# Performance work log

Measured on AMD Instinct MI355X. Metric: run time of the kernel, lower is better.

The kernel has to match this reference:

```python
import jax, jax.numpy as jnp
import numpy as np

B, IMG, P, S, D, H, HD = 64, 224, 16, 197, 768, 12, 64
MLP, L, PRUNE_AFTER, NCLS = 3072, 12, 4, 1000
N_KEEP = max(1, int(S * 0.5))  # FIXED_RATIO = 0.5 -> 98 kept tokens (plus forced CLS)


def _ln(x, w, b, eps=1e-6):
    m = x.mean(-1, keepdims=True)
    v = ((x - m) ** 2).mean(-1, keepdims=True)
    return (x - m) * jax.lax.rsqrt(v + eps) * w + b


def _block(x, ln1_w, ln1_b, qkv_w, qkv_b, proj_w, proj_b,
           ln2_w, ln2_b, fc1_w, fc1_b, fc2_w, fc2_b, key_mask=None):
    b, s, _ = x.shape
    qkv = _ln(x, ln1_w, ln1_b) @ qkv_w.T + qkv_b           # [B,S,3D]
    qkv = qkv.reshape(b, s, 3, H, HD)
    q, k, v = qkv[:, :, 0], qkv[:, :, 1], qkv[:, :, 2]     # [B,S,H,HD]
    logits = jnp.einsum('bqhd,bkhd->bhqk', q * (HD ** -0.5), k)
    if key_mask is not None:
        # masking pruned keys == varlen attention restricted to kept tokens
        logits = jnp.where(key_mask[:, None, None, :], logits, -1e9)
    attn = jax.nn.softmax(logits, axis=-1)
    out = jnp.einsum('bhqk,bkhd->bqhd', attn, v).reshape(b, s, D)
    x = x + out @ proj_w.T + proj_b
    h = _ln(x, ln2_w, ln2_b)
    h = jax.nn.gelu(h @ fc1_w.T + fc1_b, approximate=False) @ fc2_w.T + fc2_b
    return x + h


def _forward(images, patch_w, patch_b, cls_token, pos_embed,
             ln1_w, ln1_b, qkv_w, qkv_b, proj_w, proj_b,
             ln2_w, ln2_b, fc1_w, fc1_b, fc2_w, fc2_b,
             norm_w, norm_b, head_w, head_b):
    # patch embed: conv stride P == non-overlapping patch projection
    x = jax.lax.conv_general_dilated(images, patch_w, (P, P), 'VALID',
                                     dimension_numbers=('NCHW', 'OIHW', 'NCHW'))
    x = x.reshape(x.shape[0], D, -1).transpose(0, 2, 1) + patch_b       # [B,196,D]
    x = jnp.concatenate([jnp.broadcast_to(cls_token, (x.shape[0], 1, D)), x], axis=1)
    x = x + pos_embed                                                    # [B,197,D]
    for i in range(PRUNE_AFTER):
        x = _block(x, ln1_w[i], ln1_b[i], qkv_w[i], qkv_b[i], proj_w[i], proj_b[i],
                   ln2_w[i], ln2_b[i], fc1_w[i], fc1_b[i], fc2_w[i], fc2_b[i])
    # norm-score topk prune (CLS always kept), as in _threshold_prune
    scores = jnp.linalg.norm(x, axis=-1)                                 # [B,S]
    _, idx = jax.lax.top_k(scores, N_KEEP)
    mask = jnp.zeros((x.shape[0], S), bool)
    mask = mask.at[jnp.arange(x.shape[0])[:, None], idx].set(True).at[:, 0].set(True)
    # Padded-mask form of triton_pack_tokens + flash_attn_varlen: pruned tokens
    # are never attended to (masked keys) and their own outputs are unused.
    for i in range(PRUNE_AFTER, L):
        x = _block(x, ln1_w[i], ln1_b[i], qkv_w[i], qkv_b[i], proj_w[i], proj_b[i],
                   ln2_w[i], ln2_b[i], fc1_w[i], fc1_b[i], fc2_w[i], fc2_b[i],
                   key_mask=mask)
    cls = _ln(x[:, 0], norm_w, norm_b)   # packed[cu[:-1]] is always the CLS token
    return cls @ head_w.T + head_b       # [B, NCLS]


def setup_inputs():
    key = jax.random.key(0)
    ks = iter(jax.random.split(key, 32))
    def rn(shape, s=0.02):
        return jax.random.normal(next(ks), shape, jnp.float32) * s
    return {
        'images': jax.random.normal(next(ks), (B, 3, IMG, IMG), jnp.float32),
        'patch_w': rn((D, 3, P, P)), 'patch_b': jnp.zeros((D,), jnp.float32),
        'cls_token': rn((1, 1, D)), 'pos_embed': rn((1, S, D)),
        'ln1_w': jnp.ones((L, D), jnp.float32), 'ln1_b': jnp.zeros((L, D), jnp.float32),
        'qkv_w': rn((L, 3 * D, D)), 'qkv_b': jnp.zeros((L, 3 * D), jnp.float32),
        'proj_w': rn((L, D, D)), 'proj_b': jnp.zeros((L, D), jnp.float32),
        'ln2_w': jnp.ones((L, D), jnp.float32), 'ln2_b': jnp.zeros((L, D), jnp.float32),
        'fc1_w': rn((L, MLP, D)), 'fc1_b': jnp.zeros((L, MLP), jnp.float32),
        'fc2_w': rn((L, D, MLP)), 'fc2_b': jnp.zeros((L, D), jnp.float32),
        'norm_w': jnp.ones((D,), jnp.float32), 'norm_b': jnp.zeros((D,), jnp.float32),
        'head_w': rn((NCLS, D)), 'head_b': jnp.zeros((NCLS,), jnp.float32),
    }


def reference(images, patch_w, patch_b, cls_token, pos_embed,
              ln1_w, ln1_b, qkv_w, qkv_b, proj_w, proj_b,
              ln2_w, ln2_b, fc1_w, fc1_b, fc2_w, fc2_b,
              norm_w, norm_b, head_w, head_b):
    return _forward(images, patch_w, patch_b, cls_token, pos_embed,
                    ln1_w, ln1_b, qkv_w, qkv_b, proj_w, proj_b,
                    ln2_w, ln2_b, fc1_w, fc1_b, fc2_w, fc2_b,
                    norm_w, norm_b, head_w, head_b)
```

## Files before the change

### kernel.cpp

```cpp
#include <hip/hip_runtime.h>
#include <hip/hip_bf16.h>
#include <cstdint>

#define NH 12
#define SQ 197
#define DIM 768
#define HDIM 64
#define BATCH 64
#define MTOK (BATCH*SQ)
#define MLPD 3072
#define NKEEP 98
#define CSLOT 100
#define MCTOK (BATCH*CSLOT)
#define VLDF 224
#define VLDC 128

typedef __attribute__((ext_vector_type(8))) short bf16x8;
typedef __attribute__((ext_vector_type(8))) unsigned short ushort8;
typedef __attribute__((ext_vector_type(4))) unsigned short ushort4v;
typedef __attribute__((ext_vector_type(4))) float floatx4;

__device__ __forceinline__ unsigned short f2bf(float f) {
  __hip_bfloat16 h = __float2bfloat16(f);
  return reinterpret_cast<unsigned short&>(h);
}

__device__ __forceinline__ float erf_fast(float x) {
  float ax = fabsf(x);
  float t = 1.f / (1.f + 0.3275911f * ax);
  float y = t * (0.254829592f + t * (-0.284496736f + t * (1.421413741f +
            t * (-1.453152027f + t * 1.061405429f))));
  float r = 1.f - y * __expf(-ax * ax);
  return copysignf(r, x);
}

__device__ __forceinline__ void gload16(const unsigned short* g, unsigned short* l) {
  __builtin_amdgcn_global_load_lds(
      (const __attribute__((address_space(1))) void*)g,
      (__attribute__((address_space(3))) void*)l, 16, 0, 0);
}

enum { EPI_PATCH = 0, EPI_QKV = 1, EPI_RESID = 2, EPI_GELU = 3, EPI_HEAD = 4, EPI_QKVC = 5 };

template<int EPI, bool CHK, int MR, int NR>
__device__ __forceinline__ void gemm_epilogue(
    floatx4 (&acc)[MR][NR], int m0, int n0, int wr, int wc, int l15, int l4,
    const float* __restrict__ bias, int M, int N,
    float* __restrict__ xresid, const float* __restrict__ pos,
    unsigned short* __restrict__ obf, unsigned short* __restrict__ qb,
    unsigned short* __restrict__ kb, unsigned short* __restrict__ vb,
    float* __restrict__ ofp)
{
#pragma unroll
  for (int mr = 0; mr < MR; ++mr) {
#pragma unroll
    for (int nr = 0; nr < NR; ++nr) {
#pragma unroll
      for (int j = 0; j < 4; ++j) {
        int m = m0 + wr + mr * 16 + l4 * 4 + j;
        int n = n0 + wc + nr * 16 + l15;
        if (CHK && (m >= M || n >= N)) continue;
        float val = acc[mr][nr][j] + bias[n];
        if constexpr (EPI == EPI_PATCH) {
          int b = m / 196, p = m - b * 196;
          xresid[(size_t)(b * SQ + 1 + p) * DIM + n] = val + pos[(1 + p) * DIM + n];
        } else if constexpr (EPI == EPI_QKV || EPI == EPI_QKVC) {
          constexpr int SR = (EPI == EPI_QKV) ? SQ : CSLOT;
          constexpr int VL = (EPI == EPI_QKV) ? VLDF : VLDC;
          int part = n / DIM; int within = n - part * DIM;
          int h = within >> 6, hd = within & 63;
          int b = m / SR, s = m - b * SR;
          if (part == 0)      qb[(((size_t)(b * NH + h)) * SR + s) * HDIM + hd] = f2bf(val * 0.125f);
          else if (part == 1) kb[(((size_t)(b * NH + h)) * SR + s) * HDIM + hd] = f2bf(val);
          else                vb[(((size_t)(b * NH + h)) * HDIM + hd) * VL + s] = f2bf(val);
        } else if constexpr (EPI == EPI_RESID) {
          xresid[(size_t)m * DIM + n] += val;
        } else if constexpr (EPI == EPI_GELU) {
          float g = 0.5f * val * (1.f + erf_fast(val * 0.70710678118654752f));
          obf[(size_t)m * MLPD + n] = f2bf(g);
        } else {
          ofp[(size_t)m * 1000 + n] = val;
        }
      }
    }
  }
}

template<int EPI>
__global__ __launch_bounds__(512, 1)
void gemm_bf256(const unsigned short* __restrict__ A, int lda,
                const unsigned short* __restrict__ Wb, int ldw,
                const float* __restrict__ bias,
                int M, int N, int K,
                float* __restrict__ xresid,
                const float* __restrict__ pos,
                unsigned short* __restrict__ obf,
                unsigned short* __restrict__ qb,
                unsigned short* __restrict__ kb,
                unsigned short* __restrict__ vb,
                float* __restrict__ ofp)
{
  __shared__ unsigned short As[2][256 * 64];
  __shared__ unsigned short Bs[2][256 * 64];
  const int tid = threadIdx.x;
  const int lane = tid & 63;
  const int w = tid >> 6;
  const int wr = (w >> 2) * 128;
  const int wc = (w & 3) * 64;

  const int gx = gridDim.x;
  const int nwg = gx * gridDim.y;
  const int orig = blockIdx.y * gx + blockIdx.x;
  const int q = nwg >> 3, r = nwg & 7;
  const int xcd = orig & 7, o8 = orig >> 3;
  const int wgid = ((xcd < r) ? xcd * (q + 1) : r * (q + 1) + (xcd - r) * q) + o8;
  const int bx = wgid % gx, by = wgid / gx;
  const int m0 = by * 256, n0 = bx * 256;
  const int l15 = lane & 15, l4 = lane >> 4;

  const int sub = lane & 7, rsub = lane >> 3;
  const int scol = ((sub ^ rsub) << 3);
  const bool isA = (w < 4);
  const unsigned short* gp[8];
  int ldst[8];
#pragma unroll
  for (int j = 0; j < 8; ++j) {
    int row = (w & 3) * 64 + j * 8 + rsub;
    if (isA) {
      int ra = m0 + row; if (ra > M - 1) ra = M - 1;
      gp[j] = A + (size_t)ra * lda + scol;
    } else {
      int rb = n0 + row; if (rb > N - 1) rb = N - 1;
      gp[j] = Wb + (size_t)rb * ldw + scol;
    }
    ldst[j] = ((w & 3) * 8 + j) * 512;
  }

  floatx4 acc[8][4];
#pragma unroll
  for (int i = 0; i < 8; ++i)
#pragma unroll
    for (int j = 0; j < 4; ++j) acc[i][j] = {0.f, 0.f, 0.f, 0.f};

  auto STAGE = [&](int buf, int kt) {
    unsigned short* base = isA ? &As[buf][0] : &Bs[buf][0];
#pragma unroll
    for (int j = 0; j < 8; ++j)
      gload16(gp[j] + kt, base + ldst[j]);
  };

  const int nk = K >> 6;
  STAGE(0, 0);
  int cur = 0;
  for (int ki = 0; ki < nk; ++ki) {
    if (ki + 1 < nk) {
      STAGE(cur ^ 1, (ki + 1) << 6);
      asm volatile("s_waitcnt vmcnt(8)" ::: "memory");
    } else {
      asm volatile("s_waitcnt vmcnt(0)" ::: "memory");
    }
    __builtin_amdgcn_sched_barrier(0);
    __builtin_amdgcn_s_barrier();
    const unsigned short* Ac = &As[cur][0];
    const unsigned short* Bc = &Bs[cur][0];
#pragma unroll
    for (int kk = 0; kk < 2; ++kk) {
      bf16x8 af[8], bfr[4];
#pragma unroll
      for (int mr = 0; mr < 8; ++mr) {
        int row = wr + mr * 16 + l15;
        int cs = (kk * 4 + l4) ^ (row & 7);
        af[mr] = *(const bf16x8*)&Ac[row * 64 + cs * 8];
      }
#pragma unroll
      for (int nr = 0; nr < 4; ++nr) {
        int row = wc + nr * 16 + l15;
        int cs = (kk * 4 + l4) ^ (row & 7);
        bfr[nr] = *(const bf16x8*)&Bc[row * 64 + cs * 8];
      }
#pragma unroll
      for (int mr = 0; mr < 8; ++mr)
#pragma unroll
        for (int nr = 0; nr < 4; ++nr)
          acc[mr][nr] = __builtin_amdgcn_mfma_f32_16x16x32_bf16(af[mr], bfr[nr], acc[mr][nr], 0, 0, 0);
    }
    __builtin_amdgcn_sched_barrier(0);
    __builtin_amdgcn_s_barrier();
    cur ^= 1;
  }
  if (m0 + 256 <= M && n0 + 256 <= N)
    gemm_epilogue<EPI, false, 8, 4>(acc, m0, n0, wr, wc, l15, l4, bias, M, N,
                                    xresid, pos, obf, qb, kb, vb, ofp);
  else
    gemm_epilogue<EPI, true, 8, 4>(acc, m0, n0, wr, wc, l15, l4, bias, M, N,
                                   xresid, pos, obf, qb, kb, vb, ofp);
}

template<int EPI, int BN>
__global__ __launch_bounds__(256)
void gemm_bf(const unsigned short* __restrict__ A, int lda,
             const unsigned short* __restrict__ Wb, int ldw,
             const float* __restrict__ bias,
             int M, int N, int K,
             float* __restrict__ xresid,
             const float* __restrict__ pos,
             unsigned short* __restrict__ obf,
             unsigned short* __restrict__ qb,
             unsigned short* __restrict__ kb,
             unsigned short* __restrict__ vb,
             float* __restrict__ ofp)
{
  constexpr int NR = BN / 32;
  constexpr int NG = (128 + BN) / 8;
  constexpr int PG = NG / 4;
  __shared__ unsigned short As[128 * 64];
  __shared__ unsigned short Bs[BN * 64];
  const int tid = threadIdx.x;
  const int lane = tid & 63;
  const int w = tid >> 6;
  const int wr = (w >> 1) * 64, wc = (w & 1) * (BN / 2);

  const int gx = gridDim.x;
  const int nwg = gx * gridDim.y;
  const int orig = blockIdx.y * gx + blockIdx.x;
  const int q = nwg >> 3, r = nwg & 7;
  const int xcd = orig & 7, o8 = orig >> 3;
  const int wgid = ((xcd < r) ? xcd * (q + 1) : r * (q + 1) + (xcd - r) * q) + o8;
  const int bx = wgid % gx, by = wgid / gx;
  const int m0 = by * 128, n0 = bx * BN;
  const int l15 = lane & 15, l4 = lane >> 4;

  const int sub = lane & 7, rsub = lane >> 3;
  const int scol = ((sub ^ rsub) << 3);
  const unsigned short* gp[PG];
  unsigned short* lp[PG];
#pragma unroll
  for (int j = 0; j < PG; ++j) {
    int t = w * PG + j;
    if (t < 16) {
      int row = t * 8 + rsub;
      int ra = m0 + row; if (ra > M - 1) ra = M - 1;
      gp[j] = A + (size_t)ra * lda + scol;
      lp[j] = &As[t * 512];
    } else {
      int tb = t - 16;
      int row = tb * 8 + rsub;
      int rb = n0 + row; if (rb > N - 1) rb = N - 1;
      gp[j] = Wb + (size_t)rb * ldw + scol;
      lp[j] = &Bs[tb * 512];
    }
  }

  floatx4 acc[4][NR];
#pragma unroll
  for (int i = 0; i < 4; ++i)
#pragma unroll
    for (int j = 0; j < NR; ++j) acc[i][j] = {0.f, 0.f, 0.f, 0.f};

  for (int kt = 0; kt < K; kt += 64) {
#pragma unroll
    for (int j = 0; j < PG; ++j)
      gload16(gp[j] + kt, lp[j]);
    __syncthreads();
#pragma unroll
    for (int kk = 0; kk < 2; ++kk) {
      bf16x8 af[4], bfr[NR];
#pragma unroll
      for (int mr = 0; mr < 4; ++mr) {
        int row = wr + mr * 16 + l15;
        int cs = (kk * 4 + l4) ^ (row & 7);
        af[mr] = *(const bf16x8*)&As[row * 64 + cs * 8];
      }
#pragma unroll
      for (int nr = 0; nr < NR; ++nr) {
        int row = wc + nr * 16 + l15;
        int cs = (kk * 4 + l4) ^ (row & 7);
        bfr[nr] = *(const bf16x8*)&Bs[row * 64 + cs * 8];
      }
#pragma unroll
      for (int mr = 0; mr < 4; ++mr)
#pragma unroll
        for (int nr = 0; nr < NR; ++nr)
          acc[mr][nr] = __builtin_amdgcn_mfma_f32_16x16x32_bf16(af[mr], bfr[nr], acc[mr][nr], 0, 0, 0);
    }
    __syncthreads();
  }
  if (m0 + 128 <= M && n0 + BN <= N)
    gemm_epilogue<EPI, false, 4, NR>(acc, m0, n0, wr, wc, l15, l4, bias, M, N,
                                     xresid, pos, obf, qb, kb, vb, ofp);
  else
    gemm_epilogue<EPI, true, 4, NR>(acc, m0, n0, wr, wc, l15, l4, bias, M, N,
                                    xresid, pos, obf, qb, kb, vb, ofp);
}

template<int EPI>
__global__ __launch_bounds__(256)
void gemm_f32(const unsigned short* __restrict__ A, int lda,
              const float* __restrict__ Wf, int ldw,
              const float* __restrict__ bias,
              int M, int N, int K,
              float* __restrict__ xresid,
              const float* __restrict__ pos,
              unsigned short* __restrict__ obf,
              unsigned short* __restrict__ qb,
              unsigned short* __restrict__ kb,
              unsigned short* __restrict__ vb,
              float* __restrict__ ofp)
{
  __shared__ unsigned short As[128 * 64];
  __shared__ unsigned short Bs[128 * 64];
  const int tid = threadIdx.x;
  const int lane = tid & 63;
  const int w = tid >> 6;
  const int wr = (w >> 1) * 64, wc = (w & 1) * 64;
  const int m0 = blockIdx.y * 128, n0 = blockIdx.x * 128;
  const int l15 = lane & 15, l4 = lane >> 4;

  floatx4 acc[4][4];
#pragma unroll
  for (int i = 0; i < 4; ++i)
#pragma unroll
    for (int j = 0; j < 4; ++j) acc[i][j] = {0.f, 0.f, 0.f, 0.f};

  for (int kt = 0; kt < K; kt += 64) {
#pragma unroll
    for (int i = 0; i < 4; ++i) {
      int g = tid + 256 * i;
      int row = g >> 3, c = g & 7;
      int sw = (c ^ (row & 7)) * 8;
      int ra = m0 + row; if (ra > M - 1) ra = M - 1;
      ushort8 av = *(const ushort8*)(A + (size_t)ra * lda + kt + c * 8);
      *(ushort8*)&As[row * 64 + sw] = av;
      int rb = n0 + row; if (rb > N - 1) rb = N - 1;
      const float* bs = Wf + (size_t)rb * ldw + kt + c * 8;
      float4 f0 = *(const float4*)bs;
      float4 f1 = *(const float4*)(bs + 4);
      ushort8 bv;
      bv[0] = f2bf(f0.x); bv[1] = f2bf(f0.y); bv[2] = f2bf(f0.z); bv[3] = f2bf(f0.w);
      bv[4] = f2bf(f1.x); bv[5] = f2bf(f1.y); bv[6] = f2bf(f1.z); bv[7] = f2bf(f1.w);
      *(ushort8*)&Bs[row * 64 + sw] = bv;
    }
    __syncthreads();
#pragma unroll
    for (int kk = 0; kk < 2; ++kk) {
      bf16x8 af[4], bfr[4];
#pragma unroll
      for (int mr = 0; mr < 4; ++mr) {
        int row = wr + mr * 16 + l15;
        int cs = (kk * 4 + l4) ^ (row & 7);
        af[mr] = *(const bf16x8*)&As[row * 64 + cs * 8];
      }
#pragma unroll
      for (int nr = 0; nr < 4; ++nr) {
        int row = wc + nr * 16 + l15;
        int cs = (kk * 4 + l4) ^ (row & 7);
        bfr[nr] = *(const bf16x8*)&Bs[row * 64 + cs * 8];
      }
#pragma unroll
      for (int mr = 0; mr < 4; ++mr)
#pragma unroll
        for (int nr = 0; nr < 4; ++nr)
          acc[mr][nr] = __builtin_amdgcn_mfma_f32_16x16x32_bf16(af[mr], bfr[nr], acc[mr][nr], 0, 0, 0);
    }
    __syncthreads();
  }
  if (m0 + 128 <= M && n0 + 128 <= N)
    gemm_epilogue<EPI, false, 4, 4>(acc, m0, n0, wr, wc, l15, l4, bias, M, N,
                                    xresid, pos, obf, qb, kb, vb, ofp);
  else
    gemm_epilogue<EPI, true, 4, 4>(acc, m0, n0, wr, wc, l15, l4, bias, M, N,
                                   xresid, pos, obf, qb, kb, vb, ofp);
}

__global__ __launch_bounds__(256)
void cvt_kernel(const float* __restrict__ src, unsigned short* __restrict__ dst, int nchunks)
{
  int i = blockIdx.x * 256 + threadIdx.x;
  if (i >= nchunks) return;
  float4 f0 = *(const float4*)(src + (size_t)i * 8);
  float4 f1 = *(const float4*)(src + (size_t)i * 8 + 4);
  ushort8 v;
  v[0] = f2bf(f0.x); v[1] = f2bf(f0.y); v[2] = f2bf(f0.z); v[3] = f2bf(f0.w);
  v[4] = f2bf(f1.x); v[5] = f2bf(f1.y); v[6] = f2bf(f1.z); v[7] = f2bf(f1.w);
  *(ushort8*)(dst + (size_t)i * 8) = v;
}

__global__ __launch_bounds__(192)
void ln_kernel(const float* __restrict__ x, long long row_stride,
               const float* __restrict__ g, const float* __restrict__ b,
               unsigned short* __restrict__ out)
{
  int row = blockIdx.x;
  const float4* xr = (const float4*)(x + (size_t)row * row_stride);
  int t = threadIdx.x;
  float4 v = xr[t];
  float s = v.x + v.y + v.z + v.w;
  float sq = v.x * v.x + v.y * v.y + v.z * v.z + v.w * v.w;
  __shared__ float sb[6];
  for (int o = 32; o; o >>= 1) { s += __shfl_down(s, o); sq += __shfl_down(sq, o); }
  if ((t & 63) == 0) { sb[t >> 6] = s; sb[3 + (t >> 6)] = sq; }
  __syncthreads();
  s = sb[0] + sb[1] + sb[2];
  sq = sb[3] + sb[4] + sb[5];
  float mean = s * (1.f / 768.f);
  float var = sq * (1.f / 768.f) - mean * mean;
  float rstd = rsqrtf(var + 1e-6f);
  float4 gg = ((const float4*)g)[t];
  float4 bb = ((const float4*)b)[t];
  ushort4v o4;
  o4[0] = f2bf((v.x - mean) * rstd * gg.x + bb.x);
  o4[1] = f2bf((v.y - mean) * rstd * gg.y + bb.y);
  o4[2] = f2bf((v.z - mean) * rstd * gg.z + bb.z);
  o4[3] = f2bf((v.w - mean) * rstd * gg.w + bb.w);
  *(ushort4v*)(out + (size_t)row * DIM + t * 4) = o4;
}

template<int NT, int SROWS, int VLD, int PSTR, bool CNT>
__global__ __launch_bounds__(256)
void attn_kernel(const unsigned short* __restrict__ qb,
                 const unsigned short* __restrict__ kb,
                 const unsigned short* __restrict__ vb,
                 const int* __restrict__ cnt,
                 unsigned short* __restrict__ outA)
{
  __shared__ unsigned short Ks[NT * 16 * 64];
  __shared__ unsigned short Ps[4][16 * PSTR];
  int bh = blockIdx.x;
  int b = bh / NH, h = bh - b * NH;
  const int tid = threadIdx.x, lane = tid & 63, w = tid >> 6;
  const int l15 = lane & 15, l4 = lane >> 4;
  const unsigned short* kbase = kb + (size_t)bh * SROWS * HDIM;
  const unsigned short* qbase = qb + (size_t)bh * SROWS * HDIM;
  const unsigned short* vbase = vb + (size_t)bh * HDIM * VLD;
  const int limit = CNT ? cnt[b] : SROWS;

  constexpr int KCH = NT * 16 * 8;
  for (int i = 0; i < (KCH + 255) / 256; ++i) {
    int gch = tid + 256 * i;
    if (gch < KCH) {
      int row = gch >> 3, c = gch & 7;
      int rs = row > SROWS - 1 ? SROWS - 1 : row;
      ushort8 kv = *(const ushort8*)(kbase + (size_t)rs * HDIM + c * 8);
      *(ushort8*)&Ks[row * 64 + ((c ^ (row & 7))) * 8] = kv;
    }
  }
  __syncthreads();

  for (int qt = w; qt < NT; qt += 4) {
    int qrow = qt * 16 + l15; if (qrow > SROWS - 1) qrow = SROWS - 1;
    bf16x8 aq0 = *(const bf16x8*)(qbase + (size_t)qrow * HDIM + l4 * 8);
    bf16x8 aq1 = *(const bf16x8*)(qbase + (size_t)qrow * HDIM + 32 + l4 * 8);

    floatx4 lg[NT];
#pragma unroll
    for (int nt = 0; nt < NT; ++nt) {
      lg[nt] = {0.f, 0.f, 0.f, 0.f};
      int row = nt * 16 + l15;
      int cs0 = (l4) ^ (row & 7);
      int cs1 = (4 + l4) ^ (row & 7);
      bf16x8 bk0 = *(const bf16x8*)&Ks[row * 64 + cs0 * 8];
      bf16x8 bk1 = *(const bf16x8*)&Ks[row * 64 + cs1 * 8];
      lg[nt] = __builtin_amdgcn_mfma_f32_16x16x32_bf16(aq0, bk0, lg[nt], 0, 0, 0);
      lg[nt] = __builtin_amdgcn_mfma_f32_16x16x32_bf16(aq1, bk1, lg[nt], 0, 0, 0);
    }
    float mx[4] = {-1e30f, -1e30f, -1e30f, -1e30f};
#pragma unroll
    for (int nt = 0; nt < NT; ++nt) {
      int col = nt * 16 + l15;
      bool valid = col < limit;
#pragma unroll
      for (int j = 0; j < 4; ++j) {
        float v = valid ? lg[nt][j] : -1e9f;
        lg[nt][j] = v;
        mx[j] = fmaxf(mx[j], v);
      }
    }
#pragma unroll
    for (int j = 0; j < 4; ++j)
      for (int o = 1; o < 16; o <<= 1) mx[j] = fmaxf(mx[j], __shfl_xor(mx[j], o));
    float sm[4] = {0.f, 0.f, 0.f, 0.f};
#pragma unroll
    for (int nt = 0; nt < NT; ++nt)
#pragma unroll
      for (int j = 0; j < 4; ++j) {
        float p = __expf(lg[nt][j] - mx[j]);
        lg[nt][j] = p;
        sm[j] += p;
      }
#pragma unroll
    for (int j = 0; j < 4; ++j) {
      for (int o = 1; o < 16; o <<= 1) sm[j] += __shfl_xor(sm[j], o);
      sm[j] = 1.f / sm[j];
    }
    unsigned short* pw = &Ps[w][0];
#pragma unroll
    for (int nt = 0; nt < NT; ++nt) {
      int col = nt * 16 + l15;
#pragma unroll
      for (int j = 0; j < 4; ++j)
        pw[(l4 * 4 + j) * PSTR + col] = f2bf(lg[nt][j]);
    }
#pragma unroll
    for (int j = 0; j < 4; ++j)
      pw[(l4 * 4 + j) * PSTR + NT * 16 + l15] = 0;
    floatx4 oacc[4];
#pragma unroll
    for (int nr = 0; nr < 4; ++nr) oacc[nr] = {0.f, 0.f, 0.f, 0.f};
#pragma unroll
    for (int ks = 0; ks < VLD / 32; ++ks) {
      bf16x8 ap = *(const bf16x8*)&pw[l15 * PSTR + ks * 32 + l4 * 8];
#pragma unroll
      for (int nr = 0; nr < 4; ++nr) {
        bf16x8 bv = *(const bf16x8*)(vbase + (size_t)(nr * 16 + l15) * VLD + ks * 32 + l4 * 8);
        oacc[nr] = __builtin_amdgcn_mfma_f32_16x16x32_bf16(ap, bv, oacc[nr], 0, 0, 0);
      }
    }
#pragma unroll
    for (int nr = 0; nr < 4; ++nr)
#pragma unroll
      for (int j = 0; j < 4; ++j) {
        int qi = qt * 16 + l4 * 4 + j;
        if (qi < SROWS)
          outA[((size_t)(b * SROWS + qi)) * DIM + h * HDIM + nr * 16 + l15] = f2bf(oacc[nr][j] * sm[j]);
      }
  }
}

__global__ __launch_bounds__(256)
void im2col_kernel(const float* __restrict__ images, unsigned short* __restrict__ out)
{
  int idx = blockIdx.x * 256 + threadIdx.x;
  int token = idx / 96;
  int kc = (idx - token * 96) * 8;
  int b = token / 196, p = token - b * 196;
  int py = p / 14, px = p - py * 14;
  int c = kc >> 8, rem = kc & 255;
  int i = rem >> 4, j0 = rem & 15;
  const float* src = images + (((size_t)(b * 3 + c) * 224 + py * 16 + i) * 224 + px * 16 + j0);
  float4 f0 = *(const float4*)src;
  float4 f1 = *(const float4*)(src + 4);
  ushort8 v;
  v[0] = f2bf(f0.x); v[1] = f2bf(f0.y); v[2] = f2bf(f0.z); v[3] = f2bf(f0.w);
  v[4] = f2bf(f1.x); v[5] = f2bf(f1.y); v[6] = f2bf(f1.z); v[7] = f2bf(f1.w);
  *(ushort8*)(out + (size_t)token * DIM + kc) = v;
}

__global__ __launch_bounds__(256)
void clspos_kernel(const float* __restrict__ cls, const float* __restrict__ pos,
                   float* __restrict__ x)
{
  int idx = blockIdx.x * 256 + threadIdx.x;
  int b = idx / DIM, d = idx - b * DIM;
  x[(size_t)(b * SQ) * DIM + d] = cls[d] + pos[d];
}

__global__ __launch_bounds__(256)
void norms_kernel(const float* __restrict__ x, float* __restrict__ norms)
{
  int row = blockIdx.x * 4 + (threadIdx.x >> 6);
  if (row >= MTOK) return;
  int lane = threadIdx.x & 63;
  const float* xr = x + (size_t)row * DIM;
  float acc = 0.f;
  for (int d = lane; d < DIM; d += 64) { float v = xr[d]; acc += v * v; }
  for (int o = 32; o; o >>= 1) acc += __shfl_down(acc, o);
  if (lane == 0) norms[row] = acc;
}

__global__ __launch_bounds__(256)
void topk_select(const float* __restrict__ norms, short* __restrict__ sidx,
                 int* __restrict__ cntg)
{
  int b = blockIdx.x;
  __shared__ float sc[SQ];
  __shared__ unsigned char keep[SQ];
  int tid = threadIdx.x;
  if (tid < SQ) sc[tid] = norms[b * SQ + tid];
  __syncthreads();
  if (tid < SQ) {
    float mine = sc[tid];
    int rank = 0;
    for (int j = 0; j < SQ; ++j) {
      float v = sc[j];
      rank += (v > mine) || (v == mine && j < tid);
    }
    keep[tid] = (rank < NKEEP) || (tid == 0);
  }
  __syncthreads();
  if (tid == 0) {
    short* row = sidx + b * CSLOT;
    int c = 0;
    for (int s = 0; s < SQ; ++s) if (keep[s]) row[c++] = (short)s;
    cntg[b] = c;
    for (int s = c; s < CSLOT; ++s) row[s] = 0;
  }
}

__global__ __launch_bounds__(192)
void gather_kernel(const float* __restrict__ x, const short* __restrict__ sidx,
                   float* __restrict__ xc)
{
  int g = blockIdx.x;
  int b = g / CSLOT;
  int src = sidx[g];
  const float4* sp = (const float4*)(x + ((size_t)(b * SQ + src)) * DIM);
  float4* dp = (float4*)(xc + (size_t)g * DIM);
  dp[threadIdx.x] = sp[threadIdx.x];
}

template<int EPI, int BN>
static inline void launch_gemm(hipStream_t stream, bool usebf,
                               const unsigned short* A, int lda,
                               const float* Wf, const unsigned short* Wb, int ldw,
                               const float* bias, int M, int N, int K,
                               float* xresid, const float* pos,
                               unsigned short* obf, unsigned short* qb,
                               unsigned short* kb, unsigned short* vb, float* ofp)
{
  if (usebf) {
    dim3 grid((N + BN - 1) / BN, (M + 127) / 128);
    gemm_bf<EPI, BN><<<grid, 256, 0, stream>>>(A, lda, Wb, ldw, bias,
        M, N, K, xresid, pos, obf, qb, kb, vb, ofp);
  } else {
    dim3 grid((N + 127) / 128, (M + 127) / 128);
    gemm_f32<EPI><<<grid, 256, 0, stream>>>(A, lda, Wf, ldw, bias,
        M, N, K, xresid, pos, obf, qb, kb, vb, ofp);
  }
}

template<int EPI>
static inline void launch_gemm256(hipStream_t stream, bool usebf,
                                  const unsigned short* A, int lda,
                                  const float* Wf, const unsigned short* Wb, int ldw,
                                  const float* bias, int M, int N, int K,
                                  unsigned short* obf, unsigned short* qb,
                                  unsigned short* kb, unsigned short* vb)
{
  if (usebf) {
    dim3 grid(N / 256, (M + 255) / 256);
    gemm_bf256<EPI><<<grid, 512, 0, stream>>>(A, lda, Wb, ldw, bias,
        M, N, K, nullptr, nullptr, obf, qb, kb, vb, nullptr);
  } else {
    dim3 grid((N + 127) / 128, (M + 127) / 128);
    gemm_f32<EPI><<<grid, 256, 0, stream>>>(A, lda, Wf, ldw, bias,
        M, N, K, nullptr, nullptr, obf, qb, kb, vb, nullptr);
  }
}

extern "C" void kernel_launch(void* const* d_in, const int* in_sizes, int n_in,
                              void* d_out, int out_size, void* d_ws, size_t ws_size,
                              hipStream_t stream)
{
  const float* images    = (const float*)d_in[0];
  const float* patch_w   = (const float*)d_in[1];
  const float* patch_b   = (const float*)d_in[2];
  const float* cls_token = (const float*)d_in[3];
  const float* pos_embed = (const float*)d_in[4];
  const float* ln1_w = (const float*)d_in[5];
  const float* ln1_b = (const float*)d_in[6];
  const float* qkv_w = (const float*)d_in[7];
  const float* qkv_b = (const float*)d_in[8];
  const float* proj_w = (const float*)d_in[9];
  const float* proj_b = (const float*)d_in[10];
  const float* ln2_w = (const float*)d_in[11];
  const float* ln2_b = (const float*)d_in[12];
  const float* fc1_w = (const float*)d_in[13];
  const float* fc1_b = (const float*)d_in[14];
  const float* fc2_w = (const float*)d_in[15];
  const float* fc2_b = (const float*)d_in[16];
  const float* norm_w = (const float*)d_in[17];
  const float* norm_b = (const float*)d_in[18];
  const float* head_w = (const float*)d_in[19];
  const float* head_b = (const float*)d_in[20];

  char* ws = (char*)d_ws;
  size_t off = 0;
  auto alloc = [&](size_t bytes) { void* p = ws + off; off += (bytes + 255) & ~(size_t)255; return p; };
  float* x            = (float*)alloc((size_t)MTOK * DIM * 4);
  float* xc           = (float*)alloc((size_t)MCTOK * DIM * 4);
  unsigned short* xn  = (unsigned short*)alloc((size_t)MTOK * DIM * 2);
  size_t h1_bytes = (size_t)MTOK * MLPD * 2;
  unsigned short* h1  = (unsigned short*)alloc(h1_bytes);
  unsigned short* qb  = h1;
  unsigned short* kb  = qb + (size_t)BATCH * NH * SQ * HDIM;
  unsigned short* vb  = kb + (size_t)BATCH * NH * SQ * HDIM;
  size_t vbytes = (size_t)BATCH * NH * HDIM * VLDF * 2;
  unsigned short* lncls = (unsigned short*)alloc((size_t)64 * DIM * 2);
  float* norms = (float*)alloc((size_t)MTOK * 4);
  short* sidx  = (short*)alloc((size_t)MCTOK * 2);
  int* cnt = (int*)alloc(BATCH * 4);
  size_t n_qkvw = (size_t)12 * 2304 * DIM, n_projw = (size_t)12 * DIM * DIM;
  size_t n_fc1w = (size_t)12 * MLPD * DIM, n_fc2w = (size_t)12 * DIM * MLPD;
  size_t n_patw = (size_t)DIM * DIM, n_headw = (size_t)1000 * DIM;
  unsigned short* wqkv = (unsigned short*)alloc(n_qkvw * 2);
  unsigned short* wproj = (unsigned short*)alloc(n_projw * 2);
  unsigned short* wfc1 = (unsigned short*)alloc(n_fc1w * 2);
  unsigned short* wfc2 = (unsigned short*)alloc(n_fc2w * 2);
  unsigned short* wpat = (unsigned short*)alloc(n_patw * 2);
  unsigned short* whead = (unsigned short*)alloc(n_headw * 2);
  const bool usebf = (off <= ws_size);

  hipMemsetAsync(vb, 0, vbytes, stream);

  if (usebf) {
    cvt_kernel<<<(int)((n_qkvw/8 + 255)/256), 256, 0, stream>>>(qkv_w, wqkv, (int)(n_qkvw/8));
    cvt_kernel<<<(int)((n_projw/8 + 255)/256), 256, 0, stream>>>(proj_w, wproj, (int)(n_projw/8));
    cvt_kernel<<<(int)((n_fc1w/8 + 255)/256), 256, 0, stream>>>(fc1_w, wfc1, (int)(n_fc1w/8));
    cvt_kernel<<<(int)((n_fc2w/8 + 255)/256), 256, 0, stream>>>(fc2_w, wfc2, (int)(n_fc2w/8));
    cvt_kernel<<<(int)((n_patw/8 + 255)/256), 256, 0, stream>>>(patch_w, wpat, (int)(n_patw/8));
    cvt_kernel<<<(int)((n_headw/8 + 255)/256), 256, 0, stream>>>(head_w, whead, (int)(n_headw/8));
  }

  im2col_kernel<<<4704, 256, 0, stream>>>(images, h1);
  launch_gemm<EPI_PATCH, 64>(stream, usebf, h1, DIM, patch_w, wpat, DIM,
      patch_b, 12544, DIM, DIM, x, pos_embed, nullptr, nullptr, nullptr, nullptr, nullptr);
  clspos_kernel<<<192, 256, 0, stream>>>(cls_token, pos_embed, x);

  for (int l = 0; l < 4; ++l) {
    ln_kernel<<<MTOK, 192, 0, stream>>>(x, DIM, ln1_w + l * DIM, ln1_b + l * DIM, xn);
    launch_gemm256<EPI_QKV>(stream, usebf, xn, DIM,
        qkv_w + (size_t)l * 2304 * DIM, wqkv + (size_t)l * 2304 * DIM, DIM,
        qkv_b + l * 2304, MTOK, 2304, DIM, nullptr, qb, kb, vb);
    attn_kernel<13, SQ, VLDF, 248, false><<<BATCH * NH, 256, 0, stream>>>(qb, kb, vb, nullptr, xn);
    launch_gemm<EPI_RESID, 64>(stream, usebf, xn, DIM,
        proj_w + (size_t)l * DIM * DIM, wproj + (size_t)l * DIM * DIM, DIM,
        proj_b + l * DIM, MTOK, DIM, DIM, x, nullptr, nullptr, nullptr, nullptr, nullptr, nullptr);
    ln_kernel<<<MTOK, 192, 0, stream>>>(x, DIM, ln2_w + l * DIM, ln2_b + l * DIM, xn);
    launch_gemm256<EPI_GELU>(stream, usebf, xn, DIM,
        fc1_w + (size_t)l * MLPD * DIM, wfc1 + (size_t)l * MLPD * DIM, DIM,
        fc1_b + l * MLPD, MTOK, MLPD, DIM, h1, nullptr, nullptr, nullptr);
    launch_gemm<EPI_RESID, 64>(stream, usebf, h1, MLPD,
        fc2_w + (size_t)l * DIM * MLPD, wfc2 + (size_t)l * DIM * MLPD, MLPD,
        fc2_b + l * DIM, MTOK, DIM, MLPD, x, nullptr, nullptr, nullptr, nullptr, nullptr, nullptr);
  }

  norms_kernel<<<(MTOK + 3) / 4, 256, 0, stream>>>(x, norms);
  topk_select<<<BATCH, 256, 0, stream>>>(norms, sidx, cnt);
  gather_kernel<<<MCTOK, 192, 0, stream>>>(x, sidx, xc);

  for (int l = 4; l < 12; ++l) {
    ln_kernel<<<MCTOK, 192, 0, stream>>>(xc, DIM, ln1_w + l * DIM, ln1_b + l * DIM, xn);
    launch_gemm<EPI_QKVC, 128>(stream, usebf, xn, DIM,
        qkv_w + (size_t)l * 2304 * DIM, wqkv + (size_t)l * 2304 * DIM, DIM,
        qkv_b + l * 2304, MCTOK, 2304, DIM, nullptr, nullptr, nullptr, qb, kb, vb, nullptr);
    attn_kernel<7, CSLOT, VLDC, 136, true><<<BATCH * NH, 256, 0, stream>>>(qb, kb, vb, cnt, xn);
    launch_gemm<EPI_RESID, 64>(stream, usebf, xn, DIM,
        proj_w + (size_t)l * DIM * DIM, wproj + (size_t)l * DIM * DIM, DIM,
        proj_b + l * DIM, MCTOK, DIM, DIM, xc, nullptr, nullptr, nullptr, nullptr, nullptr, nullptr);
    ln_kernel<<<MCTOK, 192, 0, stream>>>(xc, DIM, ln2_w + l * DIM, ln2_b + l * DIM, xn);
    launch_gemm<EPI_GELU, 128>(stream, usebf, xn, DIM,
        fc1_w + (size_t)l * MLPD * DIM, wfc1 + (size_t)l * MLPD * DIM, DIM,
        fc1_b + l * MLPD, MCTOK, MLPD, DIM, nullptr, nullptr, h1, nullptr, nullptr, nullptr, nullptr);
    launch_gemm<EPI_RESID, 64>(stream, usebf, h1, MLPD,
        fc2_w + (size_t)l * DIM * MLPD, wfc2 + (size_t)l * DIM * MLPD, MLPD,
        fc2_b + l * DIM, MCTOK, DIM, MLPD, xc, nullptr, nullptr, nullptr, nullptr, nullptr, nullptr);
  }

  ln_kernel<<<64, 192, 0, stream>>>(xc, (long long)CSLOT * DIM, norm_w, norm_b, lncls);
  launch_gemm<EPI_HEAD, 64>(stream, usebf, lncls, DIM, head_w, whead, DIM,
      head_b, 64, 1000, DIM, nullptr, nullptr, nullptr, nullptr, nullptr, nullptr, (float*)d_out);
  (void)in_sizes; (void)n_in; (void)out_size;
}
```

Before: 3.697 ms.

## Restructure 256x256 bf16 GEMM into 4-stage K=32 pipeline with interleaved loads

Replaces the double-buffered K=64 main loop of the 256x256 bf16 GEMM with a four-slot ring of K=32 tiles, prefetching three steps ahead with a single barrier per iteration. All 512 threads now share the A and B staging instead of splitting waves into A-loaders and B-loaders. Global loads for the next A and B tiles are interleaved between two halves of the MFMA block, and s_setprio is raised around the MFMAs. The goal is to hide global-memory latency and cut barrier overhead, at the cost of halving the work done per barrier and depending on fragile manual vmcnt accounting.

```diff
diff --git a/kernel.cpp b/kernel.cpp
--- a/kernel.cpp
+++ b/kernel.cpp
@@ -88,20 +88,20 @@
 
 template<int EPI>
 __global__ __launch_bounds__(512, 1)
-void gemm_bf256(const unsigned short* __restrict__ A, int lda,
-                const unsigned short* __restrict__ Wb, int ldw,
-                const float* __restrict__ bias,
-                int M, int N, int K,
-                float* __restrict__ xresid,
-                const float* __restrict__ pos,
-                unsigned short* __restrict__ obf,
-                unsigned short* __restrict__ qb,
-                unsigned short* __restrict__ kb,
-                unsigned short* __restrict__ vb,
-                float* __restrict__ ofp)
-{
-  __shared__ unsigned short As[2][256 * 64];
-  __shared__ unsigned short Bs[2][256 * 64];
+void gemm_bf256r(const unsigned short* __restrict__ A, int lda,
+                 const unsigned short* __restrict__ Wb, int ldw,
+                 const float* __restrict__ bias,
+                 int M, int N, int K,
+                 float* __restrict__ xresid,
+                 const float* __restrict__ pos,
+                 unsigned short* __restrict__ obf,
+                 unsigned short* __restrict__ qb,
+                 unsigned short* __restrict__ kb,
+                 unsigned short* __restrict__ vb,
+                 float* __restrict__ ofp)
+{
+  __shared__ unsigned short As[4][256 * 32];
+  __shared__ unsigned short Bs[4][256 * 32];
   const int tid = threadIdx.x;
   const int lane = tid & 63;
   const int w = tid >> 6;
@@ -118,23 +118,21 @@
   const int m0 = by * 256, n0 = bx * 256;
   const int l15 = lane & 15, l4 = lane >> 4;
 
-  const int sub = lane & 7, rsub = lane >> 3;
-  const int scol = ((sub ^ rsub) << 3);
-  const bool isA = (w < 4);
-  const unsigned short* gp[8];
-  int ldst[8];
-#pragma unroll
-  for (int j = 0; j < 8; ++j) {
-    int row = (w & 3) * 64 + j * 8 + rsub;
-    if (isA) {
-      int ra = m0 + row; if (ra > M - 1) ra = M - 1;
-      gp[j] = A + (size_t)ra * lda + scol;
-    } else {
-      int rb = n0 + row; if (rb > N - 1) rb = N - 1;
-      gp[j] = Wb + (size_t)rb * ldw + scol;
-    }
-    ldst[j] = ((w & 3) * 8 + j) * 512;
-  }
+  const int srow = tid >> 2;
+  const int scol = (((tid & 3) ^ (srow & 3)) << 3);
+  int ra0 = m0 + srow;       if (ra0 > M - 1) ra0 = M - 1;
+  int ra1 = m0 + 128 + srow; if (ra1 > M - 1) ra1 = M - 1;
+  int rb0 = n0 + srow;       if (rb0 > N - 1) rb0 = N - 1;
+  int rb1 = n0 + 128 + srow; if (rb1 > N - 1) rb1 = N - 1;
+  const unsigned short* gA0 = A + (size_t)ra0 * lda + scol;
+  const unsigned short* gA1 = A + (size_t)ra1 * lda + scol;
+  const unsigned short* gB0 = Wb + (size_t)rb0 * ldw + scol;
+  const unsigned short* gB1 = Wb + (size_t)rb1 * ldw + scol;
+  const int wbase = w * 512;
+
+  const int csr = ((l4 ^ (l15 & 3)) << 3);
+  const int aoff = (wr + l15) * 32 + csr;
+  const int boff = (wc + l15) * 32 + csr;
 
   floatx4 acc[8][4];
 #pragma unroll
@@ -142,51 +140,61 @@
 #pragma unroll
     for (int j = 0; j < 4; ++j) acc[i][j] = {0.f, 0.f, 0.f, 0.f};
 
-  auto STAGE = [&](int buf, int kt) {
-    unsigned short* base = isA ? &As[buf][0] : &Bs[buf][0];
-#pragma unroll
-    for (int j = 0; j < 8; ++j)
-      gload16(gp[j] + kt, base + ldst[j]);
-  };
-
-  const int nk = K >> 6;
-  STAGE(0, 0);
-  int cur = 0;
-  for (int ki = 0; ki < nk; ++ki) {
-    if (ki + 1 < nk) {
-      STAGE(cur ^ 1, (ki + 1) << 6);
-      asm volatile("s_waitcnt vmcnt(8)" ::: "memory");
-    } else {
-      asm volatile("s_waitcnt vmcnt(0)" ::: "memory");
-    }
+  const int nk = K >> 5;
+#pragma unroll
+  for (int p = 0; p < 3; ++p) {
+    int kt = p << 5;
+    gload16(gA0 + kt, &As[p][wbase]);
+    gload16(gA1 + kt, &As[p][wbase + 4096]);
+    gload16(gB0 + kt, &Bs[p][wbase]);
+    gload16(gB1 + kt, &Bs[p][wbase + 4096]);
+  }
+
+  for (int t = 0; t < nk; ++t) {
+    const int slot = t & 3;
+    if (t < nk - 2)       asm volatile("s_waitcnt vmcnt(8)" ::: "memory");
+    else if (t == nk - 2) asm volatile("s_waitcnt vmcnt(4)" ::: "memory");
+    else                  asm volatile("s_waitcnt vmcnt(0)" ::: "memory");
     __builtin_amdgcn_sched_barrier(0);
     __builtin_amdgcn_s_barrier();
-    const unsigned short* Ac = &As[cur][0];
-    const unsigned short* Bc = &Bs[cur][0];
-#pragma unroll
-    for (int kk = 0; kk < 2; ++kk) {
-      bf16x8 af[8], bfr[4];
-#pragma unroll
-      for (int mr = 0; mr < 8; ++mr) {
-        int row = wr + mr * 16 + l15;
-        int cs = (kk * 4 + l4) ^ (row & 7);
-        af[mr] = *(const bf16x8*)&Ac[row * 64 + cs * 8];
-      }
-#pragma unroll
-      for (int nr = 0; nr < 4; ++nr) {
-        int row = wc + nr * 16 + l15;
-        int cs = (kk * 4 + l4) ^ (row & 7);
-        bfr[nr] = *(const bf16x8*)&Bc[row * 64 + cs * 8];
-      }
-#pragma unroll
-      for (int mr = 0; mr < 8; ++mr)
-#pragma unroll
-        for (int nr = 0; nr < 4; ++nr)
-          acc[mr][nr] = __builtin_amdgcn_mfma_f32_16x16x32_bf16(af[mr], bfr[nr], acc[mr][nr], 0, 0, 0);
-    }
     __builtin_amdgcn_sched_barrier(0);
-    __builtin_amdgcn_s_barrier();
-    cur ^= 1;
+    const unsigned short* Ac = &As[slot][0];
+    const unsigned short* Bc = &Bs[slot][0];
+    const bool dostage = (t + 3 < nk);
+    const int fslot = (t + 3) & 3, fkt = (t + 3) << 5;
+    if (dostage) {
+      gload16(gA0 + fkt, &As[fslot][wbase]);
+      gload16(gA1 + fkt, &As[fslot][wbase + 4096]);
+    }
+    bf16x8 af[8], bfr[4];
+#pragma unroll
+    for (int nr = 0; nr < 4; ++nr) bfr[nr] = *(const bf16x8*)&Bc[boff + nr * 512];
+#pragma unroll
+    for (int mr = 0; mr < 4; ++mr) af[mr] = *(const bf16x8*)&Ac[aoff + mr * 512];
+    asm volatile("s_waitcnt lgkmcnt(0)" ::: "memory");
+    __builtin_amdgcn_sched_barrier(0);
+    __builtin_amdgcn_s_setprio(1);
+#pragma unroll
+    for (int mr = 0; mr < 4; ++mr)
+#pragma unroll
+      for (int nr = 0; nr < 4; ++nr)
+        acc[mr][nr] = __builtin_amdgcn_mfma_f32_16x16x32_bf16(af[mr], bfr[nr], acc[mr][nr], 0, 0, 0);
+    __builtin_amdgcn_s_setprio(0);
+    if (dostage) {
+      gload16(gB0 + fkt, &Bs[fslot][wbase]);
+      gload16(gB1 + fkt, &Bs[fslot][wbase + 4096]);
+    }
+#pragma unroll
+    for (int mr = 4; mr < 8; ++mr) af[mr] = *(const bf16x8*)&Ac[aoff + mr * 512];
+    asm volatile("s_waitcnt lgkmcnt(0)" ::: "memory");
+    __builtin_amdgcn_sched_barrier(0);
+    __builtin_amdgcn_s_setprio(1);
+#pragma unroll
+    for (int mr = 4; mr < 8; ++mr)
+#pragma unroll
+      for (int nr = 0; nr < 4; ++nr)
+        acc[mr][nr] = __builtin_amdgcn_mfma_f32_16x16x32_bf16(af[mr], bfr[nr], acc[mr][nr], 0, 0, 0);
+    __builtin_amdgcn_s_setprio(0);
   }
   if (m0 + 256 <= M && n0 + 256 <= N)
     gemm_epilogue<EPI, false, 8, 4>(acc, m0, n0, wr, wc, l15, l4, bias, M, N,
@@ -638,7 +646,7 @@
 {
   if (usebf) {
     dim3 grid(N / 256, (M + 255) / 256);
-    gemm_bf256<EPI><<<grid, 512, 0, stream>>>(A, lda, Wb, ldw, bias,
+    gemm_bf256r<EPI><<<grid, 512, 0, stream>>>(A, lda, Wb, ldw, bias,
         M, N, K, nullptr, nullptr, obf, qb, kb, vb, nullptr);
   } else {
     dim3 grid((N + 127) / 128, (M + 127) / 128);
```

Result: no change. 3.765 ms (+1.9%).
